# Performance work log

Hardware: AMD Instinct MI355X
Metric: run time of the kernel (lower is better)

The kernel has to match this reference:

```python
import jax, jax.numpy as jnp
import numpy as np

N_NODES = 100000
N_EDGES = 1600000
C = 64            # in_channels == out_channels
EC = 32           # edge_channels


def setup_inputs() -> dict:
    key = jax.random.key(0)
    ks = jax.random.split(key, 8)
    s = 1.0 / np.sqrt(C)
    x = jax.random.normal(ks[0], (N_NODES, C), dtype=jnp.float32)
    edge_index = jax.random.randint(ks[1], (2, N_EDGES), 0, N_NODES, dtype=jnp.int64)
    edge_attr = jax.random.normal(ks[2], (N_EDGES, EC), dtype=jnp.float32)
    We = jax.random.uniform(ks[3], (C, EC), minval=-1/np.sqrt(EC), maxval=1/np.sqrt(EC), dtype=jnp.float32)  # edge_lin weight
    W = jax.random.uniform(ks[4], (C, C), minval=-s, maxval=s, dtype=jnp.float32)   # GatedGraphConv weight[0]
    W_ih = jax.random.uniform(ks[5], (3 * C, C), minval=-s, maxval=s, dtype=jnp.float32)
    W_hh = jax.random.uniform(ks[6], (3 * C, C), minval=-s, maxval=s, dtype=jnp.float32)
    b_ih = jnp.zeros((3 * C,), dtype=jnp.float32)
    b_hh = jnp.zeros((3 * C,), dtype=jnp.float32)
    return {"x": x, "edge_index": edge_index, "edge_attr": edge_attr,
            "We": We, "W": W, "W_ih": W_ih, "W_hh": W_hh, "b_ih": b_ih, "b_hh": b_hh}


def reference(x, edge_index, edge_attr, We, W, W_ih, W_hh, b_ih, b_hh):
    n_nodes = x.shape[0]
    # edge_lin: [E, EC] -> [E, C]
    ew = edge_attr @ We.T
    # GatedGraphConv, num_layers=1, aggr='add'
    m = x @ W                                  # [N, C]
    src, dst = edge_index[0], edge_index[1]
    msg = m[src] * ew                          # gather + elementwise edge weight, [E, C]
    agg = jax.ops.segment_sum(msg, dst, num_segments=n_nodes)  # scatter-add
    # GRUCell(agg, x)
    gi = agg @ W_ih.T + b_ih                   # [N, 3C]
    gh = x @ W_hh.T + b_hh                     # [N, 3C]
    i_r, i_z, i_n = jnp.split(gi, 3, axis=-1)
    h_r, h_z, h_n = jnp.split(gh, 3, axis=-1)
    r = jax.nn.sigmoid(i_r + h_r)
    z = jax.nn.sigmoid(i_z + h_z)
    n = jnp.tanh(i_n + r * h_n)
    h = (1.0 - z) * n + z * x
    out = jax.nn.relu(h)
    # residual blend, alpha = 0.5, res_lin = Identity (in == out channels)
    return 0.5 * out + 0.5 * x
```

## Files before the change

kernel.cpp:

```cpp
#include <hip/hip_runtime.h>
#include <math.h>

#define NN 100000
#define NE 1600000
#define CC 64
#define CAP 64
#define NBXW ((NN + 63) / 64)
#define GFRONT 2048

typedef unsigned int uint;
typedef _Float16 f16;
typedef _Float16 h2 __attribute__((ext_vector_type(2)));
typedef _Float16 f16x8 __attribute__((ext_vector_type(8)));
typedef float f32x4 __attribute__((ext_vector_type(4)));

__device__ __forceinline__ uint pk2(float a, float b) {
    f16 x = (f16)a, y = (f16)b;
    return (uint)__builtin_bit_cast(unsigned short, x) |
           ((uint)__builtin_bit_cast(unsigned short, y) << 16);
}

__global__ __launch_bounds__(256) void k_front(const float* __restrict__ x,
                                               const float* __restrict__ W,
                                               const int* __restrict__ ei,
                                               const float* __restrict__ ea,
                                               f16* __restrict__ mh,
                                               f16* __restrict__ xh,
                                               uint4* __restrict__ eah4,
                                               int* __restrict__ cnt,
                                               int2* __restrict__ pe_pad) {
    __shared__ float xs[64][64];
    __shared__ float wsm[64][64];
    const int b = blockIdx.x;
    const int t = threadIdx.x;

    {
        int i = b * 256 + t;
        const int stride = GFRONT * 256;
        for (int e = i; e < NE; e += stride) {
            int d = ei[NE + e];
            int s = ei[e];
            int old = atomicAdd(&cnt[d], 1);
            if (old < CAP)
                pe_pad[(size_t)d * CAP + old] = make_int2(e, s);
        }
    }
    {
        const float4* ea4 = (const float4*)ea;
        const int total = NE * 4;
        int i = b * 256 + t;
        const int stride = GFRONT * 256;
        for (; i < total; i += stride) {
            float4 a = ea4[2 * (size_t)i];
            float4 c = ea4[2 * (size_t)i + 1];
            eah4[i] = make_uint4(pk2(a.x, a.y), pk2(a.z, a.w),
                                 pk2(c.x, c.y), pk2(c.z, c.w));
        }
    }
    if (b < NBXW) {
        const int j = t & 63;
        const int g = t >> 6;
        const int base = b * 64;
        const int jperm = (j & 15) * 4 + (j >> 4);
#pragma unroll
        for (int r = 0; r < 16; ++r) {
            int idx = r * 256 + t;
            wsm[idx >> 6][idx & 63] = W[idx];
        }
#pragma unroll
        for (int r = 0; r < 16; ++r) {
            int idx = r * 256 + t;
            int n = idx >> 6, k = idx & 63;
            int gi = base + n;
            float v = 0.f;
            if (gi < NN) {
                v = x[(size_t)gi * 64 + k];
                xh[(size_t)gi * 64 + k] = (f16)v;
            }
            xs[n][k] = v;
        }
        __syncthreads();
        float acc[16];
#pragma unroll
        for (int q = 0; q < 16; ++q) acc[q] = 0.f;
        for (int k = 0; k < 64; ++k) {
            float w = wsm[k][j];
#pragma unroll
            for (int q = 0; q < 16; ++q)
                acc[q] = fmaf(xs[g * 16 + q][k], w, acc[q]);
        }
#pragma unroll
        for (int q = 0; q < 16; ++q) {
            int n = base + g * 16 + q;
            if (n < NN) mh[(size_t)n * 64 + jperm] = (f16)acc[q];
        }
    }
}

__global__ __launch_bounds__(256) void k_agg(const int* __restrict__ cnt,
                                             const int2* __restrict__ pe_pad,
                                             const f16* __restrict__ eah,
                                             const f16* __restrict__ mh2,
                                             const float* __restrict__ We,
                                             f16* __restrict__ aggh) {
    const int t = threadIdx.x;
    const int lane = t & 63;
    const int wv = t >> 6;
    const int p = lane & 15;
    const int g = lane >> 4;
    f16x8 bf0, bf1, bf2, bf3;
    {
        const float* w0 = We + (0 * 16 + p) * 32 + g * 8;
        const float* w1 = We + (1 * 16 + p) * 32 + g * 8;
        const float* w2 = We + (2 * 16 + p) * 32 + g * 8;
        const float* w3 = We + (3 * 16 + p) * 32 + g * 8;
#pragma unroll
        for (int j = 0; j < 8; ++j) {
            bf0[j] = (f16)w0[j]; bf1[j] = (f16)w1[j];
            bf2[j] = (f16)w2[j]; bf3[j] = (f16)w3[j];
        }
    }
    const int wid = blockIdx.x * 4 + wv;
    const int nw = gridDim.x * 4;
    for (int n = wid; n < NN; n += nw) {
        int deg = cnt[n];
        deg = (deg > CAP) ? CAP : deg;
        const int2* bin = pe_pad + (size_t)n * CAP;
        float acc0 = 0.f, acc1 = 0.f, acc2 = 0.f, acc3 = 0.f;
        for (int s0 = 0; s0 < deg; s0 += 16) {
            int nb = deg - s0; nb = (nb > 16) ? 16 : nb;
            int2 v = bin[s0 + (p < nb ? p : 0)];
            f16x8 af = *(const f16x8*)(eah + (size_t)v.x * 32 + g * 8);
            int srcv = v.y;
            f32x4 c0 = {0.f, 0.f, 0.f, 0.f};
            f32x4 c1 = {0.f, 0.f, 0.f, 0.f};
            f32x4 c2 = {0.f, 0.f, 0.f, 0.f};
            f32x4 c3 = {0.f, 0.f, 0.f, 0.f};
            c0 = __builtin_amdgcn_mfma_f32_16x16x32_f16(af, bf0, c0, 0, 0, 0);
            c1 = __builtin_amdgcn_mfma_f32_16x16x32_f16(af, bf1, c1, 0, 0, 0);
            c2 = __builtin_amdgcn_mfma_f32_16x16x32_f16(af, bf2, c2, 0, 0, 0);
            c3 = __builtin_amdgcn_mfma_f32_16x16x32_f16(af, bf3, c3, 0, 0, 0);
#pragma unroll
            for (int r = 0; r < 4; ++r) {
                int er = g * 4 + r;
                int src = __shfl(srcv, er);
                uint2 md = *(const uint2*)(mh2 + (size_t)src * 64 + p * 4);
                h2 mlo = __builtin_bit_cast(h2, md.x);
                h2 mhi = __builtin_bit_cast(h2, md.y);
                float m0 = (float)mlo[0], m1 = (float)mlo[1];
                float m2 = (float)mhi[0], m3 = (float)mhi[1];
                if (er >= nb) { m0 = 0.f; m1 = 0.f; m2 = 0.f; m3 = 0.f; }
                acc0 = fmaf(c0[r], m0, acc0);
                acc1 = fmaf(c1[r], m1, acc1);
                acc2 = fmaf(c2[r], m2, acc2);
                acc3 = fmaf(c3[r], m3, acc3);
            }
        }
        acc0 += __shfl_xor(acc0, 16); acc0 += __shfl_xor(acc0, 32);
        acc1 += __shfl_xor(acc1, 16); acc1 += __shfl_xor(acc1, 32);
        acc2 += __shfl_xor(acc2, 16); acc2 += __shfl_xor(acc2, 32);
        acc3 += __shfl_xor(acc3, 16); acc3 += __shfl_xor(acc3, 32);
        float v = (g == 0) ? acc0 : (g == 1) ? acc1 : (g == 2) ? acc2 : acc3;
        aggh[(size_t)n * 64 + lane] = (f16)v;
    }
}

__global__ __launch_bounds__(256) void k_gru(const f16* __restrict__ aggh,
                                             const f16* __restrict__ xh,
                                             const float* __restrict__ Wih,
                                             const float* __restrict__ Whh,
                                             const float* __restrict__ bih,
                                             const float* __restrict__ bhh,
                                             float* __restrict__ out) {
    __shared__ f16 wl[192 * 136];
    const int t = threadIdx.x;
    const int lane = t & 63;
    const int wv = t >> 6;
    const int p = lane & 15;
    const int g = lane >> 4;
#pragma unroll
    for (int i = 0; i < 48; ++i) {
        int idx = i * 256 + t;
        int c = idx >> 6, k = idx & 63;
        wl[c * 136 + k] = (f16)Wih[idx];
        wl[c * 136 + 64 + k] = (f16)Whh[idx];
    }
    float bihv[12], bhhv[12];
#pragma unroll
    for (int i = 0; i < 12; ++i) {
        bihv[i] = bih[i * 16 + p];
        bhhv[i] = bhh[i * 16 + p];
    }
    __syncthreads();
    const int wid = blockIdx.x * 4 + wv;
    const int nw = gridDim.x * 4;
    for (int b = wid; b < NN / 16; b += nw) {
        const f16* ar = aggh + (size_t)b * 16 * 64;
        const f16* xr = xh + (size_t)b * 16 * 64;
        const int ro = p * 64 + g * 8;
        f16x8 a0 = *(const f16x8*)(ar + ro);
        f16x8 a1 = *(const f16x8*)(ar + ro + 32);
        f16x8 x0 = *(const f16x8*)(xr + ro);
        f16x8 x1 = *(const f16x8*)(xr + ro + 32);
#pragma unroll
        for (int nt = 0; nt < 4; ++nt) {
            const f16* w0 = wl + (nt * 16 + p) * 136 + g * 8;
            const f16* w1 = wl + ((nt + 4) * 16 + p) * 136 + g * 8;
            const f16* w2 = wl + ((nt + 8) * 16 + p) * 136 + g * 8;
            f32x4 cir = {0.f, 0.f, 0.f, 0.f};
            f32x4 ciz = {0.f, 0.f, 0.f, 0.f};
            f32x4 cin = {0.f, 0.f, 0.f, 0.f};
            f32x4 chr_ = {0.f, 0.f, 0.f, 0.f};
            f32x4 chz = {0.f, 0.f, 0.f, 0.f};
            f32x4 chn = {0.f, 0.f, 0.f, 0.f};
            cir = __builtin_amdgcn_mfma_f32_16x16x32_f16(a0, *(const f16x8*)(w0), cir, 0, 0, 0);
            cir = __builtin_amdgcn_mfma_f32_16x16x32_f16(a1, *(const f16x8*)(w0 + 32), cir, 0, 0, 0);
            ciz = __builtin_amdgcn_mfma_f32_16x16x32_f16(a0, *(const f16x8*)(w1), ciz, 0, 0, 0);
            ciz = __builtin_amdgcn_mfma_f32_16x16x32_f16(a1, *(const f16x8*)(w1 + 32), ciz, 0, 0, 0);
            cin = __builtin_amdgcn_mfma_f32_16x16x32_f16(a0, *(const f16x8*)(w2), cin, 0, 0, 0);
            cin = __builtin_amdgcn_mfma_f32_16x16x32_f16(a1, *(const f16x8*)(w2 + 32), cin, 0, 0, 0);
            chr_ = __builtin_amdgcn_mfma_f32_16x16x32_f16(x0, *(const f16x8*)(w0 + 64), chr_, 0, 0, 0);
            chr_ = __builtin_amdgcn_mfma_f32_16x16x32_f16(x1, *(const f16x8*)(w0 + 96), chr_, 0, 0, 0);
            chz = __builtin_amdgcn_mfma_f32_16x16x32_f16(x0, *(const f16x8*)(w1 + 64), chz, 0, 0, 0);
            chz = __builtin_amdgcn_mfma_f32_16x16x32_f16(x1, *(const f16x8*)(w1 + 96), chz, 0, 0, 0);
            chn = __builtin_amdgcn_mfma_f32_16x16x32_f16(x0, *(const f16x8*)(w2 + 64), chn, 0, 0, 0);
            chn = __builtin_amdgcn_mfma_f32_16x16x32_f16(x1, *(const f16x8*)(w2 + 96), chn, 0, 0, 0);
            int c = nt * 16 + p;
#pragma unroll
            for (int r4 = 0; r4 < 4; ++r4) {
                int node = b * 16 + g * 4 + r4;
                float pr = cir[r4] + bihv[nt] + chr_[r4] + bhhv[nt];
                float pz = ciz[r4] + bihv[nt + 4] + chz[r4] + bhhv[nt + 4];
                float tin = cin[r4] + bihv[nt + 8];
                float thn = chn[r4] + bhhv[nt + 8];
                float rr = 1.f / (1.f + __expf(-pr));
                float zz = 1.f / (1.f + __expf(-pz));
                float tt = tin + rr * thn;
                float nn = 2.f / (1.f + __expf(-2.f * tt)) - 1.f;
                float xv = (float)xh[(size_t)node * 64 + c];
                float h = (1.f - zz) * nn + zz * xv;
                float o = h > 0.f ? h : 0.f;
                out[(size_t)node * 64 + c] = 0.5f * o + 0.5f * xv;
            }
        }
    }
}

extern "C" void kernel_launch(void* const* d_in, const int* in_sizes, int n_in,
                              void* d_out, int out_size, void* d_ws, size_t ws_size,
                              hipStream_t stream) {
    const float* x   = (const float*)d_in[0];
    const int*   ei  = (const int*)d_in[1];
    const float* ea  = (const float*)d_in[2];
    const float* We  = (const float*)d_in[3];
    const float* W   = (const float*)d_in[4];
    const float* Wih = (const float*)d_in[5];
    const float* Whh = (const float*)d_in[6];
    const float* bih = (const float*)d_in[7];
    const float* bhh = (const float*)d_in[8];
    float* out = (float*)d_out;

    char* ws = (char*)d_ws;
    f16* mh = (f16*)ws;
    size_t off = ((size_t)NN * CC * 2 + 255) & ~(size_t)255;
    f16* xh   = (f16*)(ws + off); off += ((size_t)NN * CC * 2 + 255) & ~(size_t)255;
    f16* aggh = (f16*)(ws + off); off += ((size_t)NN * CC * 2 + 255) & ~(size_t)255;
    f16* eah  = (f16*)(ws + off); off += (size_t)NE * 32 * 2;
    int2* pe_pad = (int2*)(ws + off); off += (size_t)NN * CAP * 8;
    int* cnt  = (int*)(ws + off); off += (size_t)NN * 4;

    (void)in_sizes; (void)n_in; (void)out_size; (void)ws_size;

    hipMemsetAsync(cnt, 0, (size_t)NN * sizeof(int), stream);
    k_front<<<GFRONT, 256, 0, stream>>>(x, W, ei, ea, mh, xh,
                                        (uint4*)eah, cnt, pe_pad);
    k_agg<<<4096, 256, 0, stream>>>(cnt, pe_pad, eah, mh, We, aggh);
    k_gru<<<768, 256, 0, stream>>>(aggh, xh, Wih, Whh, bih, bhh, out);
}
```

Before: 297.4 us.

## Replace global-atomic edge bucketing with two-pass coarse bucket sort

Edge-to-destination bucketing moves out of the front kernel into two new kernels. The first builds per-tile local histograms over 1024-node coarse buckets and reserves global ranges with one atomic per bucket. The second scatters each bucket into the padded per-node lists using shared-memory atomics. This replaces 1.6M scattered global atomics on random destinations with mostly shared-memory atomics. The cost is an extra pass over the edge records, two more launches, and a fixed per-bucket capacity (RCAP) that silently drops edges if a bucket overflows.

```diff
diff --git a/kernel.cpp b/kernel.cpp
--- a/kernel.cpp
+++ b/kernel.cpp
@@ -6,9 +6,13 @@
 #define CC 64
 #define CAP 64
 #define NBXW ((NN + 63) / 64)
-#define GFRONT 2048
+#define GXWT 2048
+#define NBK 98
+#define RCAP 17664
+#define NTILES ((NE + 2047) / 2048)
 
 typedef unsigned int uint;
+typedef unsigned char uchar;
 typedef _Float16 f16;
 typedef _Float16 h2 __attribute__((ext_vector_type(2)));
 typedef _Float16 f16x8 __attribute__((ext_vector_type(8)));
@@ -20,37 +24,21 @@
            ((uint)__builtin_bit_cast(unsigned short, y) << 16);
 }
 
-__global__ __launch_bounds__(256) void k_front(const float* __restrict__ x,
-                                               const float* __restrict__ W,
-                                               const int* __restrict__ ei,
-                                               const float* __restrict__ ea,
-                                               f16* __restrict__ mh,
-                                               f16* __restrict__ xh,
-                                               uint4* __restrict__ eah4,
-                                               int* __restrict__ cnt,
-                                               int2* __restrict__ pe_pad) {
+__global__ __launch_bounds__(256) void k_xWt(const float* __restrict__ x,
+                                             const float* __restrict__ W,
+                                             const float* __restrict__ ea,
+                                             f16* __restrict__ mh,
+                                             f16* __restrict__ xh,
+                                             uint4* __restrict__ eah4) {
     __shared__ float xs[64][64];
     __shared__ float wsm[64][64];
     const int b = blockIdx.x;
     const int t = threadIdx.x;
-
-    {
-        int i = b * 256 + t;
-        const int stride = GFRONT * 256;
-        for (int e = i; e < NE; e += stride) {
-            int d = ei[NE + e];
-            int s = ei[e];
-            int old = atomicAdd(&cnt[d], 1);
-            if (old < CAP)
-                pe_pad[(size_t)d * CAP + old] = make_int2(e, s);
-        }
-    }
     {
         const float4* ea4 = (const float4*)ea;
         const int total = NE * 4;
-        int i = b * 256 + t;
-        const int stride = GFRONT * 256;
-        for (; i < total; i += stride) {
+        const int stride = GXWT * 256;
+        for (int i = b * 256 + t; i < total; i += stride) {
             float4 a = ea4[2 * (size_t)i];
             float4 c = ea4[2 * (size_t)i + 1];
             eah4[i] = make_uint4(pk2(a.x, a.y), pk2(a.z, a.w),
@@ -95,6 +83,91 @@
             if (n < NN) mh[(size_t)n * 64 + jperm] = (f16)acc[q];
         }
     }
+}
+
+__global__ __launch_bounds__(256) void k_bktA(const int* __restrict__ ei,
+                                              int* __restrict__ gcur,
+                                              uint2* __restrict__ recs) {
+    __shared__ int hist[NBK];
+    __shared__ int lstart[NBK];
+    __shared__ int gstart[NBK];
+    __shared__ uint2 lrec[2048];
+    __shared__ uchar lbk[2048];
+    const int t = threadIdx.x;
+    const int tbase = blockIdx.x * 2048;
+    const int tn = (NE - tbase < 2048) ? (NE - tbase) : 2048;
+    for (int i = t; i < NBK; i += 256) hist[i] = 0;
+    __syncthreads();
+    int myE[8], myS[8], myRank[8], myBk[8], myDl[8];
+#pragma unroll
+    for (int k = 0; k < 8; ++k) {
+        int idx = t + k * 256;
+        myBk[k] = -1;
+        if (idx < tn) {
+            int e = tbase + idx;
+            int d = ei[NE + e];
+            myS[k] = ei[e];
+            myE[k] = e;
+            myBk[k] = d >> 10;
+            myDl[k] = d & 1023;
+            myRank[k] = atomicAdd(&hist[myBk[k]], 1);
+        }
+    }
+    __syncthreads();
+    if (t == 0) {
+        int run = 0;
+        for (int b2 = 0; b2 < NBK; ++b2) { lstart[b2] = run; run += hist[b2]; }
+    }
+    __syncthreads();
+    if (t < NBK) {
+        int c = hist[t];
+        gstart[t] = (c > 0) ? atomicAdd(&gcur[t], c) : 0;
+    }
+    __syncthreads();
+#pragma unroll
+    for (int k = 0; k < 8; ++k) {
+        if (myBk[k] >= 0) {
+            int lpos = lstart[myBk[k]] + myRank[k];
+            lrec[lpos] = make_uint2(((uint)myE[k] << 10) | (uint)myDl[k],
+                                    (uint)myS[k]);
+            lbk[lpos] = (uchar)myBk[k];
+        }
+    }
+    __syncthreads();
+    for (int lpos = t; lpos < tn; lpos += 256) {
+        int bk = lbk[lpos];
+        int idx = gstart[bk] + (lpos - lstart[bk]);
+        if (idx < RCAP)
+            recs[(size_t)bk * RCAP + idx] = lrec[lpos];
+    }
+}
+
+__global__ __launch_bounds__(1024) void k_bktB(const uint2* __restrict__ recs,
+                                               const int* __restrict__ gcur,
+                                               int* __restrict__ cnt,
+                                               int2* __restrict__ pe_pad) {
+    __shared__ int lcnt[1024];
+    const int b = blockIdx.x;
+    const int t = threadIdx.x;
+    lcnt[t] = 0;
+    __syncthreads();
+    const int base_node = b << 10;
+    int nrec = gcur[b];
+    if (nrec > RCAP) nrec = RCAP;
+    const uint2* rb = recs + (size_t)b * RCAP;
+    for (int i = t; i < nrec; i += 1024) {
+        uint2 r = rb[i];
+        int dloc = r.x & 1023;
+        int e = (int)(r.x >> 10);
+        int slot = atomicAdd(&lcnt[dloc], 1);
+        if (slot < CAP) {
+            int node = base_node + dloc;
+            pe_pad[(size_t)node * CAP + slot] = make_int2(e, (int)r.y);
+        }
+    }
+    __syncthreads();
+    int node = base_node + t;
+    if (node < NN) cnt[node] = lcnt[t];
 }
 
 __global__ __launch_bounds__(256) void k_agg(const int* __restrict__ cnt,
@@ -267,13 +340,16 @@
     f16* aggh = (f16*)(ws + off); off += ((size_t)NN * CC * 2 + 255) & ~(size_t)255;
     f16* eah  = (f16*)(ws + off); off += (size_t)NE * 32 * 2;
     int2* pe_pad = (int2*)(ws + off); off += (size_t)NN * CAP * 8;
-    int* cnt  = (int*)(ws + off); off += (size_t)NN * 4;
+    uint2* recs = (uint2*)(ws + off); off += (size_t)NBK * RCAP * 8;
+    int* cnt  = (int*)(ws + off); off += ((size_t)NN * 4 + 255) & ~(size_t)255;
+    int* gcur = (int*)(ws + off); off += (size_t)NBK * 4;
 
     (void)in_sizes; (void)n_in; (void)out_size; (void)ws_size;
 
-    hipMemsetAsync(cnt, 0, (size_t)NN * sizeof(int), stream);
-    k_front<<<GFRONT, 256, 0, stream>>>(x, W, ei, ea, mh, xh,
-                                        (uint4*)eah, cnt, pe_pad);
+    hipMemsetAsync(gcur, 0, NBK * sizeof(int), stream);
+    k_xWt<<<GXWT, 256, 0, stream>>>(x, W, ea, mh, xh, (uint4*)eah);
+    k_bktA<<<NTILES, 256, 0, stream>>>(ei, gcur, recs);
+    k_bktB<<<NBK, 1024, 0, stream>>>(recs, gcur, cnt, pe_pad);
     k_agg<<<4096, 256, 0, stream>>>(cnt, pe_pad, eah, mh, We, aggh);
     k_gru<<<768, 256, 0, stream>>>(aggh, xh, Wih, Whh, bih, bhh, out);
 }
```

After: 261.6 us. 1.14x faster.
